# Kernel optimization log

Hardware: AMD Instinct MI355X
Metric: run time of the kernel (lower is better)

The kernel has to match this reference:

```python
import jax, jax.numpy as jnp
import numpy as np

KG_E = 200000
IN_DIM = 256
OUT_DIM = 128
B = 20000
N_RAND = 620000  # random edges; self-loops appended -> total 640000


def setup_inputs() -> dict:
    key = jax.random.key(0)
    ks = jax.random.split(key, 8)
    ent_embed = jax.random.normal(ks[0], (KG_E, IN_DIM), dtype=jnp.float32)
    batch_ids = jax.random.randint(ks[1], (B,), 0, KG_E, dtype=jnp.int64)
    # random edges: rows are batch-local [0,B), cols are global [0,KG_E)
    rand_rows = jax.random.randint(ks[2], (N_RAND,), 0, B, dtype=jnp.int64)
    rand_cols = jax.random.randint(ks[3], (N_RAND,), 0, KG_E, dtype=jnp.int64)
    # self-loops as in drop_neigh: row=node_num, col=batch_ids
    rows = jnp.concatenate([rand_rows, jnp.arange(B, dtype=jnp.int64)])
    cols = jnp.concatenate([rand_cols, batch_ids])
    edge_index = jnp.stack([rows, cols])  # [2, E]
    W = jax.random.normal(ks[4], (OUT_DIM, IN_DIM), dtype=jnp.float32) * (1.0 / np.sqrt(IN_DIM))
    b = jax.random.normal(ks[5], (OUT_DIM,), dtype=jnp.float32) * 0.01
    w_atten_r = jax.random.normal(ks[6], (2 * OUT_DIM, 1), dtype=jnp.float32) * 0.1
    prelu_w = jnp.full((1,), 0.25, dtype=jnp.float32)
    return {"ent_embed": ent_embed, "batch_ids": batch_ids, "edge_index": edge_index,
            "W": W, "b": b, "w_atten_r": w_atten_r, "prelu_w": prelu_w}


def reference(ent_embed, batch_ids, edge_index, W, b, w_atten_r, prelu_w):
    # gat_in = Linear(ent_embed): [KG_E, out]
    gat_in = ent_embed @ W.T + b
    rows = edge_index[0]  # batch-local [0,B)
    cols = edge_index[1]  # global [0,KG_E)
    left = gat_in[batch_ids[rows]]   # [E, out]  (left_embed[edge_index[0]])
    right = gat_in[cols]             # [E, out]
    # concat([left,right]) @ w_atten_r  ==  left@w_a[:out] + right@w_a[out:]
    score = (left @ w_atten_r[:OUT_DIM] + right @ w_atten_r[OUT_DIM:])[:, 0]  # [E]
    att = jnp.exp(-jax.nn.leaky_relu(score, negative_slope=0.2))
    nB = batch_ids.shape[0]
    # special_spmm with ones(KG_E,1): per-row sum of attention
    e_rowsum = jax.ops.segment_sum(att, rows, num_segments=nB)  # [B]
    # special_spmm with gat_in: attention-weighted neighbor aggregation
    e_out = jax.ops.segment_sum(att[:, None] * right, rows, num_segments=nB)  # [B, out]
    e_out = e_out / e_rowsum[:, None]
    # PReLU with single learnable scalar
    return jnp.where(e_out >= 0, e_out, prelu_w[0] * e_out)
```

## Files before the change

kernel.cpp:

```cpp
#include <hip/hip_runtime.h>

#define KG_E   200000
#define IN_DIM 256
#define OUT_DIM 128
#define BATCH  20000
#define NEDGE  640000

typedef unsigned short ushort_t;
typedef __attribute__((ext_vector_type(8))) short bf16x8;
typedef __attribute__((ext_vector_type(4))) float f32x4;

__device__ __forceinline__ float bf2f(unsigned int u) {
  return __builtin_bit_cast(float, u << 16);
}
__device__ __forceinline__ unsigned short f2bf(float f) {
  unsigned int x = __builtin_bit_cast(unsigned int, f);
  x += 0x7FFFu + ((x >> 16) & 1u);
  return (unsigned short)(x >> 16);
}
__device__ __forceinline__ int idx_at(const void* p, long long i, int is64) {
  return is64 ? (int)((const long long*)p)[i] : ((const int*)p)[i];
}
__device__ __forceinline__ float fld(const void* p, int i, int isf32) {
  return isf32 ? ((const float*)p)[i] : bf2f(((const ushort_t*)p)[i]);
}
__device__ __forceinline__ bf16x8 pack8(f32x4 a, f32x4 b) {
  bf16x8 r;
#pragma unroll
  for (int j = 0; j < 4; j++) {
    ((ushort_t*)&r)[j]     = f2bf(a[j]);
    ((ushort_t*)&r)[4 + j] = f2bf(b[j]);
  }
  return r;
}

__global__ __launch_bounds__(64) void detect_kernel(const void* __restrict__ ent,
                                                    const void* __restrict__ edge,
                                                    int* __restrict__ flags) {
  int lane = threadIdx.x;
  const ushort_t* u = (const ushort_t*)ent;
  int plaus = 0;
#pragma unroll
  for (int i = 0; i < 4; i++) {
    int e = (u[2 * (lane * 4 + i)] >> 7) & 0xff;
    if (e >= 113 && e <= 141) plaus++;
  }
  const int* ei = (const int*)edge;
  int nz = (ei[2 * lane + 1] != 0) ? 1 : 0;
#pragma unroll
  for (int m = 32; m >= 1; m >>= 1) {
    plaus += __shfl_xor(plaus, m);
    nz    += __shfl_xor(nz, m);
  }
  if (lane == 0) {
    flags[0] = (plaus >= 128) ? 0 : 1;
    flags[1] = (nz == 0) ? 1 : 0;
  }
}

__global__ __launch_bounds__(512, 4) void gemm_kernel(
    const void* __restrict__ ent, const void* __restrict__ W,
    const void* __restrict__ bias, const void* __restrict__ w_atten,
    const int* __restrict__ flags, ushort_t* __restrict__ gat,
    float* __restrict__ sRn, float* __restrict__ sLn)
{
  __shared__ __align__(16) unsigned char lds[65536];
  const int isf32 = flags[0];
  const int tid  = threadIdx.x;
  const int lane = tid & 63;
  const int w    = tid >> 6;
  const int l16  = lane & 15;
  const int quad = lane >> 4;
  const int m0   = blockIdx.x * 128;

#pragma unroll
  for (int i = 0; i < 8; i++) {
    int L = i * 512 + tid;
    int r = L >> 5, s = L & 31;
    bf16x8 v;
    if (isf32) {
      const float* bp = (const float*)W + r * 256 + s * 8;
      v = pack8(*(const f32x4*)bp, *(const f32x4*)(bp + 4));
    } else {
      v = *(const bf16x8*)((const ushort_t*)W + r * 256 + s * 8);
    }
    *(bf16x8*)(lds + r * 512 + ((s ^ (r & 15)) * 16)) = v;
  }
  __syncthreads();

  const int row0 = m0 + w * 16;
  int arow = row0 + l16; arow = arow < KG_E ? arow : (KG_E - 1);

  f32x4 acc[8];
#pragma unroll
  for (int nt = 0; nt < 8; nt++) acc[nt] = (f32x4){0.f, 0.f, 0.f, 0.f};

#define MFMA_STEP(AF, KS)                                                     \
  do {                                                                        \
    _Pragma("unroll") for (int nt = 0; nt < 8; nt++) {                        \
      bf16x8 bf = *(const bf16x8*)(lds + (nt * 16 + l16) * 512 +              \
                                   ((((KS) * 4 + quad) ^ l16) * 16));         \
      acc[nt] = __builtin_amdgcn_mfma_f32_16x16x32_bf16(AF, bf, acc[nt], 0, 0, 0); \
    }                                                                         \
  } while (0)

  if (isf32) {
    const float* ap = (const float*)ent + (size_t)arow * IN_DIM + quad * 8;
    f32x4 b0[4], b1[4];
#pragma unroll
    for (int p = 0; p < 4; p++) {
      b0[p] = *(const f32x4*)(ap + p * 32);
      b1[p] = *(const f32x4*)(ap + p * 32 + 4);
    }
#pragma unroll
    for (int ks = 0; ks < 8; ks++) {
      bf16x8 af = pack8(b0[ks & 3], b1[ks & 3]);
      if (ks < 4) {
        b0[ks & 3] = *(const f32x4*)(ap + (ks + 4) * 32);
        b1[ks & 3] = *(const f32x4*)(ap + (ks + 4) * 32 + 4);
      }
      MFMA_STEP(af, ks);
    }
  } else {
    const ushort_t* ap = (const ushort_t*)ent + (size_t)arow * IN_DIM + quad * 8;
    bf16x8 ab[4];
#pragma unroll
    for (int p = 0; p < 4; p++) ab[p] = *(const bf16x8*)(ap + p * 32);
#pragma unroll
    for (int ks = 0; ks < 8; ks++) {
      bf16x8 af = ab[ks & 3];
      if (ks < 4) ab[ks & 3] = *(const bf16x8*)(ap + (ks + 4) * 32);
      MFMA_STEP(af, ks);
    }
  }
#undef MFMA_STEP

  float bv[8], w1v[8], w2v[8];
#pragma unroll
  for (int nt = 0; nt < 8; nt++) {
    int c = nt * 16 + l16;
    bv[nt]  = fld(bias, c, isf32);
    w1v[nt] = fld(w_atten, c, isf32);
    w2v[nt] = fld(w_atten, OUT_DIM + c, isf32);
  }
  float pr[4] = {0.f, 0.f, 0.f, 0.f}, pl[4] = {0.f, 0.f, 0.f, 0.f};
#pragma unroll
  for (int nt = 0; nt < 8; nt++)
#pragma unroll
    for (int reg = 0; reg < 4; reg++) {
      float v = acc[nt][reg] + bv[nt];
      acc[nt][reg] = v;
      pr[reg] += v * w2v[nt];
      pl[reg] += v * w1v[nt];
    }
#pragma unroll
  for (int m = 1; m < 16; m <<= 1)
#pragma unroll
    for (int reg = 0; reg < 4; reg++) {
      pr[reg] += __shfl_xor(pr[reg], m);
      pl[reg] += __shfl_xor(pl[reg], m);
    }
  if (l16 == 0) {
#pragma unroll
    for (int reg = 0; reg < 4; reg++) {
      int r = row0 + quad * 4 + reg;
      if (r < KG_E) { sRn[r] = pr[reg]; sLn[r] = pl[reg]; }
    }
  }

  __syncthreads();
#pragma unroll
  for (int nt = 0; nt < 8; nt++)
#pragma unroll
    for (int reg = 0; reg < 4; reg++)
      *(ushort_t*)(lds + (w * 16 + quad * 4 + reg) * 272 + (nt * 16 + l16) * 2) =
          f2bf(acc[nt][reg]);
  __syncthreads();
#pragma unroll
  for (int i = 0; i < 4; i++) {
    int L = i * 512 + tid;
    int rl = L >> 4, cs = L & 15;
    int gr = m0 + rl;
    if (gr < KG_E) {
      f32x4 v = *(const f32x4*)(lds + rl * 272 + cs * 16);
      *(f32x4*)((char*)gat + (size_t)gr * 256 + cs * 16) = v;
    }
  }
}

__global__ __launch_bounds__(256) void hist_kernel(const void* __restrict__ edge,
                                                   const int* __restrict__ flags,
                                                   int* __restrict__ counts)
{
  int is64 = flags[1];
  int e = blockIdx.x * 256 + threadIdx.x;
  if (e < NEDGE) {
    int r = idx_at(edge, e, is64);
    r = r < 0 ? 0 : (r >= BATCH ? BATCH - 1 : r);
    atomicAdd(&counts[r], 1);
  }
}

__global__ __launch_bounds__(1024) void scan1_kernel(const int* __restrict__ counts,
                                                     int* __restrict__ offsets,
                                                     int* __restrict__ blocksums)
{
  __shared__ int buf[1024];
  int i = blockIdx.x * 1024 + threadIdx.x;
  int v = (i < BATCH) ? counts[i] : 0;
  buf[threadIdx.x] = v;
  __syncthreads();
  for (int off = 1; off < 1024; off <<= 1) {
    int t = (threadIdx.x >= (unsigned)off) ? buf[threadIdx.x - off] : 0;
    __syncthreads();
    buf[threadIdx.x] += t;
    __syncthreads();
  }
  if (i < BATCH) offsets[i] = buf[threadIdx.x] - v;
  if (threadIdx.x == 1023) blocksums[blockIdx.x] = buf[1023];
}

__global__ __launch_bounds__(64) void scan2_kernel(const int* __restrict__ blocksums,
                                                   int* __restrict__ blockoff,
                                                   int* __restrict__ offsets)
{
  int lane = threadIdx.x;
  int v = (lane < 20) ? blocksums[lane] : 0;
  int orig = v;
#pragma unroll
  for (int off = 1; off < 32; off <<= 1) {
    int t = __shfl_up(v, off);
    if (lane >= off) v += t;
  }
  if (lane < 20) blockoff[lane] = v - orig;
  if (lane == 19) offsets[BATCH] = v;
}

__global__ __launch_bounds__(1024) void scan3_kernel(int* __restrict__ offsets,
                                                     const int* __restrict__ blockoff,
                                                     int* __restrict__ cursor)
{
  int i = blockIdx.x * 1024 + threadIdx.x;
  if (i < BATCH) {
    int o = offsets[i] + blockoff[blockIdx.x];
    offsets[i] = o;
    cursor[i] = o;
  }
}

__global__ __launch_bounds__(256) void scatter_kernel(const void* __restrict__ edge,
                                                      const int* __restrict__ flags,
                                                      int* __restrict__ cursor,
                                                      int* __restrict__ perm)
{
  int is64 = flags[1];
  int e = blockIdx.x * 256 + threadIdx.x;
  if (e < NEDGE) {
    int r = idx_at(edge, e, is64);
    r = r < 0 ? 0 : (r >= BATCH ? BATCH - 1 : r);
    int p = atomicAdd(&cursor[r], 1);
    perm[p] = e;
  }
}

__global__ __launch_bounds__(256) void aggregate_kernel(
    const ushort_t* __restrict__ gat, const void* __restrict__ edge,
    const int* __restrict__ perm, const int* __restrict__ offsets,
    const float* __restrict__ sRn, const float* __restrict__ sLn,
    const void* __restrict__ batch_ids, const void* __restrict__ prelu,
    const int* __restrict__ flags, float* __restrict__ out)
{
  int isf32 = flags[0], is64 = flags[1];
  int row  = blockIdx.x * 4 + (threadIdx.x >> 6);
  int lane = threadIdx.x & 63;
  int beg = offsets[row], end = offsets[row + 1];
  int b = idx_at(batch_ids, row, is64);
  b = b < 0 ? 0 : (b >= KG_E ? KG_E - 1 : b);
  float sLi = sLn[b];
  float acc0 = 0.f, acc1 = 0.f, rowsum = 0.f;
  for (int base = beg; base < end; base += 64) {
    int n = end - base; n = n < 64 ? n : 64;
    float att_l = 0.f;
    int col_l = 0;
    if (base + lane < end) {
      int e = perm[base + lane];
      int c = idx_at(edge, (long long)NEDGE + e, is64);
      col_l = c < 0 ? 0 : (c >= KG_E ? KG_E - 1 : c);
      float score = sLi + sRn[col_l];
      float lr = score > 0.f ? score : 0.2f * score;
      lr = lr > 80.f ? 80.f : (lr < -80.f ? -80.f : lr);
      att_l = __expf(-lr);
    }
    int j = 0;
    for (; j + 4 <= n; j += 4) {
      float a0 = __shfl(att_l, j),     a1 = __shfl(att_l, j + 1);
      float a2 = __shfl(att_l, j + 2), a3 = __shfl(att_l, j + 3);
      int c0 = __shfl(col_l, j),     c1 = __shfl(col_l, j + 1);
      int c2 = __shfl(col_l, j + 2), c3 = __shfl(col_l, j + 3);
      unsigned int p0 = *(const unsigned int*)(gat + (size_t)c0 * OUT_DIM + 2 * lane);
      unsigned int p1 = *(const unsigned int*)(gat + (size_t)c1 * OUT_DIM + 2 * lane);
      unsigned int p2 = *(const unsigned int*)(gat + (size_t)c2 * OUT_DIM + 2 * lane);
      unsigned int p3 = *(const unsigned int*)(gat + (size_t)c3 * OUT_DIM + 2 * lane);
      acc0 += a0 * bf2f(p0 & 0xffffu) + a1 * bf2f(p1 & 0xffffu) +
              a2 * bf2f(p2 & 0xffffu) + a3 * bf2f(p3 & 0xffffu);
      acc1 += a0 * bf2f(p0 >> 16) + a1 * bf2f(p1 >> 16) +
              a2 * bf2f(p2 >> 16) + a3 * bf2f(p3 >> 16);
      rowsum += a0 + a1 + a2 + a3;
    }
    for (; j < n; ++j) {
      float att = __shfl(att_l, j);
      int col   = __shfl(col_l, j);
      unsigned int pk = *(const unsigned int*)(gat + (size_t)col * OUT_DIM + 2 * lane);
      acc0 += att * bf2f(pk & 0xffffu);
      acc1 += att * bf2f(pk >> 16);
      rowsum += att;
    }
  }
  float inv = rowsum > 0.f ? 1.0f / rowsum : 0.f;
  float pw = fld(prelu, 0, isf32);
  float v0 = acc0 * inv, v1 = acc1 * inv;
  v0 = v0 >= 0.f ? v0 : pw * v0;
  v1 = v1 >= 0.f ? v1 : pw * v1;
  *(float2*)(out + (size_t)row * OUT_DIM + 2 * lane) = make_float2(v0, v1);
}

extern "C" void kernel_launch(void* const* d_in, const int* in_sizes, int n_in,
                              void* d_out, int out_size, void* d_ws, size_t ws_size,
                              hipStream_t stream) {
  const void* ent       = d_in[0];
  const void* batch_ids = d_in[1];
  const void* edge      = d_in[2];
  const void* W         = d_in[3];
  const void* bias      = d_in[4];
  const void* w_atten   = d_in[5];
  const void* prelu     = d_in[6];
  float*      out       = (float*)d_out;

  char* p = (char*)d_ws;
  int* flags     = (int*)p;       p += 64;
  ushort_t* gat  = (ushort_t*)p;  p += (size_t)KG_E * OUT_DIM * 2;
  float* sRn     = (float*)p;     p += (size_t)KG_E * 4;
  float* sLn     = (float*)p;     p += (size_t)KG_E * 4;
  int* counts    = (int*)p;       p += (size_t)BATCH * 4;
  int* offsets   = (int*)p;       p += (size_t)(BATCH + 1) * 4;
  int* cursor    = (int*)p;       p += (size_t)BATCH * 4;
  int* blocksums = (int*)p;       p += 64 * 4;
  int* blockoff  = (int*)p;       p += 64 * 4;
  int* perm      = (int*)p;       p += (size_t)NEDGE * 4;

  hipMemsetAsync(counts, 0, BATCH * sizeof(int), stream);
  detect_kernel<<<dim3(1), dim3(64), 0, stream>>>(ent, edge, flags);
  gemm_kernel<<<dim3((KG_E + 127) / 128), dim3(512), 0, stream>>>(
      ent, W, bias, w_atten, flags, gat, sRn, sLn);
  hist_kernel<<<dim3(NEDGE / 256), dim3(256), 0, stream>>>(edge, flags, counts);
  scan1_kernel<<<dim3(20), dim3(1024), 0, stream>>>(counts, offsets, blocksums);
  scan2_kernel<<<dim3(1), dim3(64), 0, stream>>>(blocksums, blockoff, offsets);
  scan3_kernel<<<dim3(20), dim3(1024), 0, stream>>>(offsets, blockoff, cursor);
  scatter_kernel<<<dim3(NEDGE / 256), dim3(256), 0, stream>>>(edge, flags, cursor, perm);
  aggregate_kernel<<<dim3(BATCH / 4), dim3(256), 0, stream>>>(
      gat, edge, perm, offsets, sRn, sLn, batch_ids, prelu, flags, out);
}
```

Measured before the change: 436.7 us.

## Compute attention in scatter pass and store packed (col, att) in CSR order

```diff
diff --git a/kernel.cpp b/kernel.cpp
--- a/kernel.cpp
+++ b/kernel.cpp
@@ -238,83 +238,81 @@
 
 __global__ __launch_bounds__(1024) void scan3_kernel(int* __restrict__ offsets,
                                                      const int* __restrict__ blockoff,
-                                                     int* __restrict__ cursor)
-{
+                                                     int* __restrict__ cursor,
+                                                     const void* __restrict__ batch_ids,
+                                                     const float* __restrict__ sLn,
+                                                     const int* __restrict__ flags,
+                                                     float* __restrict__ sLrow)
+{
+  int is64 = flags[1];
   int i = blockIdx.x * 1024 + threadIdx.x;
   if (i < BATCH) {
     int o = offsets[i] + blockoff[blockIdx.x];
     offsets[i] = o;
     cursor[i] = o;
+    int b = idx_at(batch_ids, i, is64);
+    b = b < 0 ? 0 : (b >= KG_E ? KG_E - 1 : b);
+    sLrow[i] = sLn[b];
   }
 }
 
 __global__ __launch_bounds__(256) void scatter_kernel(const void* __restrict__ edge,
                                                       const int* __restrict__ flags,
+                                                      const float* __restrict__ sLrow,
+                                                      const float* __restrict__ sRn,
                                                       int* __restrict__ cursor,
-                                                      int* __restrict__ perm)
+                                                      int2* __restrict__ colatt)
 {
   int is64 = flags[1];
   int e = blockIdx.x * 256 + threadIdx.x;
   if (e < NEDGE) {
     int r = idx_at(edge, e, is64);
     r = r < 0 ? 0 : (r >= BATCH ? BATCH - 1 : r);
+    int c = idx_at(edge, (long long)NEDGE + e, is64);
+    c = c < 0 ? 0 : (c >= KG_E ? KG_E - 1 : c);
+    float score = sLrow[r] + sRn[c];
+    float lr = score > 0.f ? score : 0.2f * score;
+    lr = lr > 80.f ? 80.f : (lr < -80.f ? -80.f : lr);
+    float att = __expf(-lr);
     int p = atomicAdd(&cursor[r], 1);
-    perm[p] = e;
+    colatt[p] = make_int2(c, __builtin_bit_cast(int, att));
   }
 }
 
 __global__ __launch_bounds__(256) void aggregate_kernel(
-    const ushort_t* __restrict__ gat, const void* __restrict__ edge,
-    const int* __restrict__ perm, const int* __restrict__ offsets,
-    const float* __restrict__ sRn, const float* __restrict__ sLn,
-    const void* __restrict__ batch_ids, const void* __restrict__ prelu,
+    const ushort_t* __restrict__ gat, const int2* __restrict__ colatt,
+    const int* __restrict__ offsets, const void* __restrict__ prelu,
     const int* __restrict__ flags, float* __restrict__ out)
 {
-  int isf32 = flags[0], is64 = flags[1];
-  int row  = blockIdx.x * 4 + (threadIdx.x >> 6);
+  int isf32 = flags[0];
+  int row  = __builtin_amdgcn_readfirstlane(blockIdx.x * 4 + (threadIdx.x >> 6));
   int lane = threadIdx.x & 63;
-  int beg = offsets[row], end = offsets[row + 1];
-  int b = idx_at(batch_ids, row, is64);
-  b = b < 0 ? 0 : (b >= KG_E ? KG_E - 1 : b);
-  float sLi = sLn[b];
+  int beg = __builtin_amdgcn_readfirstlane(offsets[row]);
+  int end = __builtin_amdgcn_readfirstlane(offsets[row + 1]);
   float acc0 = 0.f, acc1 = 0.f, rowsum = 0.f;
-  for (int base = beg; base < end; base += 64) {
-    int n = end - base; n = n < 64 ? n : 64;
-    float att_l = 0.f;
-    int col_l = 0;
-    if (base + lane < end) {
-      int e = perm[base + lane];
-      int c = idx_at(edge, (long long)NEDGE + e, is64);
-      col_l = c < 0 ? 0 : (c >= KG_E ? KG_E - 1 : c);
-      float score = sLi + sRn[col_l];
-      float lr = score > 0.f ? score : 0.2f * score;
-      lr = lr > 80.f ? 80.f : (lr < -80.f ? -80.f : lr);
-      att_l = __expf(-lr);
-    }
-    int j = 0;
-    for (; j + 4 <= n; j += 4) {
-      float a0 = __shfl(att_l, j),     a1 = __shfl(att_l, j + 1);
-      float a2 = __shfl(att_l, j + 2), a3 = __shfl(att_l, j + 3);
-      int c0 = __shfl(col_l, j),     c1 = __shfl(col_l, j + 1);
-      int c2 = __shfl(col_l, j + 2), c3 = __shfl(col_l, j + 3);
-      unsigned int p0 = *(const unsigned int*)(gat + (size_t)c0 * OUT_DIM + 2 * lane);
-      unsigned int p1 = *(const unsigned int*)(gat + (size_t)c1 * OUT_DIM + 2 * lane);
-      unsigned int p2 = *(const unsigned int*)(gat + (size_t)c2 * OUT_DIM + 2 * lane);
-      unsigned int p3 = *(const unsigned int*)(gat + (size_t)c3 * OUT_DIM + 2 * lane);
-      acc0 += a0 * bf2f(p0 & 0xffffu) + a1 * bf2f(p1 & 0xffffu) +
-              a2 * bf2f(p2 & 0xffffu) + a3 * bf2f(p3 & 0xffffu);
-      acc1 += a0 * bf2f(p0 >> 16) + a1 * bf2f(p1 >> 16) +
-              a2 * bf2f(p2 >> 16) + a3 * bf2f(p3 >> 16);
-      rowsum += a0 + a1 + a2 + a3;
-    }
-    for (; j < n; ++j) {
-      float att = __shfl(att_l, j);
-      int col   = __shfl(col_l, j);
-      unsigned int pk = *(const unsigned int*)(gat + (size_t)col * OUT_DIM + 2 * lane);
-      acc0 += att * bf2f(pk & 0xffffu);
-      acc1 += att * bf2f(pk >> 16);
-      rowsum += att;
-    }
+  int j = beg;
+  for (; j + 4 <= end; j += 4) {
+    int2 q0 = colatt[j],     q1 = colatt[j + 1];
+    int2 q2 = colatt[j + 2], q3 = colatt[j + 3];
+    float a0 = __builtin_bit_cast(float, q0.y), a1 = __builtin_bit_cast(float, q1.y);
+    float a2 = __builtin_bit_cast(float, q2.y), a3 = __builtin_bit_cast(float, q3.y);
+    unsigned int p0 = *(const unsigned int*)(gat + (size_t)q0.x * OUT_DIM + 2 * lane);
+    unsigned int p1 = *(const unsigned int*)(gat + (size_t)q1.x * OUT_DIM + 2 * lane);
+    unsigned int p2 = *(const unsigned int*)(gat + (size_t)q2.x * OUT_DIM + 2 * lane);
+    unsigned int p3 = *(const unsigned int*)(gat + (size_t)q3.x * OUT_DIM + 2 * lane);
+    acc0 += a0 * bf2f(p0 & 0xffffu) + a1 * bf2f(p1 & 0xffffu) +
+            a2 * bf2f(p2 & 0xffffu) + a3 * bf2f(p3 & 0xffffu);
+    acc1 += a0 * bf2f(p0 >> 16) + a1 * bf2f(p1 >> 16) +
+            a2 * bf2f(p2 >> 16) + a3 * bf2f(p3 >> 16);
+    rowsum += a0 + a1 + a2 + a3;
+  }
+  for (; j < end; ++j) {
+    int2 q = colatt[j];
+    float a = __builtin_bit_cast(float, q.y);
+    unsigned int pk = *(const unsigned int*)(gat + (size_t)q.x * OUT_DIM + 2 * lane);
+    acc0 += a * bf2f(pk & 0xffffu);
+    acc1 += a * bf2f(pk >> 16);
+    rowsum += a;
   }
   float inv = rowsum > 0.f ? 1.0f / rowsum : 0.f;
   float pw = fld(prelu, 0, isf32);
@@ -341,12 +339,14 @@
   ushort_t* gat  = (ushort_t*)p;  p += (size_t)KG_E * OUT_DIM * 2;
   float* sRn     = (float*)p;     p += (size_t)KG_E * 4;
   float* sLn     = (float*)p;     p += (size_t)KG_E * 4;
+  float* sLrow   = (float*)p;     p += (size_t)BATCH * 4;
   int* counts    = (int*)p;       p += (size_t)BATCH * 4;
   int* offsets   = (int*)p;       p += (size_t)(BATCH + 1) * 4;
   int* cursor    = (int*)p;       p += (size_t)BATCH * 4;
   int* blocksums = (int*)p;       p += 64 * 4;
   int* blockoff  = (int*)p;       p += 64 * 4;
-  int* perm      = (int*)p;       p += (size_t)NEDGE * 4;
+  p = (char*)(((size_t)p + 15) & ~(size_t)15);
+  int2* colatt   = (int2*)p;      p += (size_t)NEDGE * 8;
 
   hipMemsetAsync(counts, 0, BATCH * sizeof(int), stream);
   detect_kernel<<<dim3(1), dim3(64), 0, stream>>>(ent, edge, flags);
@@ -355,8 +355,10 @@
   hist_kernel<<<dim3(NEDGE / 256), dim3(256), 0, stream>>>(edge, flags, counts);
   scan1_kernel<<<dim3(20), dim3(1024), 0, stream>>>(counts, offsets, blocksums);
   scan2_kernel<<<dim3(1), dim3(64), 0, stream>>>(blocksums, blockoff, offsets);
-  scan3_kernel<<<dim3(20), dim3(1024), 0, stream>>>(offsets, blockoff, cursor);
-  scatter_kernel<<<dim3(NEDGE / 256), dim3(256), 0, stream>>>(edge, flags, cursor, perm);
+  scan3_kernel<<<dim3(20), dim3(1024), 0, stream>>>(offsets, blockoff, cursor,
+                                                    batch_ids, sLn, flags, sLrow);
+  scatter_kernel<<<dim3(NEDGE / 256), dim3(256), 0, stream>>>(
+      edge, flags, sLrow, sRn, cursor, colatt);
   aggregate_kernel<<<dim3(BATCH / 4), dim3(256), 0, stream>>>(
-      gat, edge, perm, offsets, sRn, sLn, batch_ids, prelu, flags, out);
-}
+      gat, colatt, offsets, prelu, flags, out);
+}
```

After: 431.0 us. No clear change (-1.3%).
